# Kernel optimization log

Hardware: AMD Instinct MI355X
Metric: run time of the kernel (lower is better)

## Reference

```python
import jax, jax.numpy as jnp
import numpy as np

N, D, NUM_CLASSES = 8192, 256, 64
MARGIN_SAME = 0.9
MARGIN_DIFF = 0.5


def setup_inputs() -> dict:
    key = jax.random.key(0)
    k1, k2 = jax.random.split(key)
    inputs = jax.random.normal(k1, (N, D), dtype=jnp.float32)
    # contrastive losses with cosine-style margins expect unit-norm embeddings
    inputs = inputs / jnp.linalg.norm(inputs, axis=1, keepdims=True)
    targets = jax.random.randint(k2, (N,), 0, NUM_CLASSES, dtype=jnp.int64)
    return {"inputs": inputs, "targets": targets}


def reference(inputs, targets):
    n = inputs.shape[0]
    sim = jnp.matmul(inputs, inputs.T)  # [n, n] pairwise similarities

    same = targets[:, None] == targets[None, :]  # [n, n]
    pos_mask = same & (sim < 1.0)                # pos_pair_ selection per row
    neg_mask = ~same                             # neg_pair_ selection per row

    pos_active = pos_mask & (sim < MARGIN_SAME)  # contribute 1 - sim
    neg_active = neg_mask & (sim > MARGIN_DIFF)  # contribute sim

    # sum over all rows, divided by n (sort in the original is irrelevant to sums)
    loss = (jnp.sum(jnp.where(pos_active, 1.0 - sim, 0.0))
            + jnp.sum(jnp.where(neg_active, sim, 0.0))) / n

    prec = jnp.float32(0.0)  # original: c is never incremented

    # original reports means of the LAST row's pos_pair_ / neg_pair_
    last_sim = sim[n - 1]
    lp = pos_mask[n - 1]
    ln = neg_mask[n - 1]
    mean_pos_sim = jnp.sum(jnp.where(lp, last_sim, 0.0)) / jnp.maximum(
        jnp.sum(lp).astype(jnp.float32), 1.0)
    mean_neg_sim = jnp.sum(jnp.where(ln, last_sim, 0.0)) / jnp.maximum(
        jnp.sum(ln).astype(jnp.float32), 1.0)

    return (loss, prec, mean_pos_sim, mean_neg_sim)
```

## Files before the change

kernel.cpp:

```cpp
#include <hip/hip_runtime.h>
#include <hip/hip_bf16.h>

#define N_ 8192
#define D_ 256
#define BM 128
#define BK 32
#define NB (N_ / BM)
#define NT (NB * (NB + 1) / 2)
#define KSTEPS (D_ / BK)

typedef __bf16 bf16x8 __attribute__((ext_vector_type(8)));
typedef float f32x4 __attribute__((ext_vector_type(4)));

__global__ void cvt_kernel(const float4* __restrict__ in, ushort4* __restrict__ out, int n4,
                           double* __restrict__ accd) {
  int i = blockIdx.x * blockDim.x + threadIdx.x;
  if (blockIdx.x == 0 && threadIdx.x < 128) accd[threadIdx.x] = 0.0;
  if (i >= n4) return;
  float4 v = in[i];
  union { __hip_bfloat16 h[4]; ushort4 u; } t;
  t.h[0] = __float2bfloat16(v.x);
  t.h[1] = __float2bfloat16(v.y);
  t.h[2] = __float2bfloat16(v.z);
  t.h[3] = __float2bfloat16(v.w);
  out[i] = t.u;
}

__global__ __launch_bounds__(256, 3) void simloss_kernel(
    const __hip_bfloat16* __restrict__ Xb, const int* __restrict__ tg,
    double* __restrict__ accd) {
  __shared__ __align__(16) char lds[3 * 16384];

  const int t0 = blockIdx.x;
  const int t = (t0 & 7) * (NT / 8) + (t0 >> 3);

  int bi = (int)(((2.0f * NB + 1.0f) -
                  sqrtf((2.0f * NB + 1.0f) * (2.0f * NB + 1.0f) - 8.0f * (float)t)) * 0.5f);
  if (bi < 0) bi = 0;
  if (bi > NB - 1) bi = NB - 1;
  while (((bi + 1) * NB - ((bi + 1) * bi) / 2) <= t) ++bi;
  while ((bi * NB - (bi * (bi - 1)) / 2) > t) --bi;
  const int bj = bi + (t - (bi * NB - (bi * (bi - 1)) / 2));

  const int tid = threadIdx.x;
  const int lane = tid & 63, wv = tid >> 6;
  const int wr = wv >> 1, wc = wv & 1;
  const int rowA0 = bi * BM, rowB0 = bj * BM;

  const int c0 = (wv * 2 + 0) * 64 + lane;
  const int c1 = (wv * 2 + 1) * 64 + lane;
  const int r0 = c0 >> 2, s0 = (c0 & 3) ^ ((r0 >> 1) & 3);
  const int r1 = c1 >> 2, s1 = (c1 & 3) ^ ((r1 >> 1) & 3);
  const __hip_bfloat16* gA0 = Xb + (size_t)(rowA0 + r0) * D_ + s0 * 8;
  const __hip_bfloat16* gA1 = Xb + (size_t)(rowA0 + r1) * D_ + s1 * 8;
  const __hip_bfloat16* gB0 = Xb + (size_t)(rowB0 + r0) * D_ + s0 * 8;
  const __hip_bfloat16* gB1 = Xb + (size_t)(rowB0 + r1) * D_ + s1 * 8;

#define GLDS(g, l) \
  __builtin_amdgcn_global_load_lds((const __attribute__((address_space(1))) void*)(g), \
                                   (__attribute__((address_space(3))) void*)(l), 16, 0, 0)
#define STAGE(buf, kt)                                    \
  do {                                                    \
    char* base = lds + (buf) * 16384;                     \
    GLDS(gA0 + (kt) * BK, base + c0 * 16);                \
    GLDS(gA1 + (kt) * BK, base + c1 * 16);                \
    GLDS(gB0 + (kt) * BK, base + 8192 + c0 * 16);         \
    GLDS(gB1 + (kt) * BK, base + 8192 + c1 * 16);         \
  } while (0)

  const int fr = lane & 15, sl = lane >> 4;
  const int rswz = sl ^ ((fr >> 1) & 3);
  const int aoff = (wr * 64 + fr) * 64 + rswz * 16;
  const int boff = (wc * 64 + fr) * 64 + rswz * 16;

  f32x4 acc[4][4] = {};

  STAGE(0, 0);
  STAGE(1, 1);
  STAGE(2, 2);

#pragma unroll
  for (int kt = 0; kt < KSTEPS; ++kt) {
    if (kt < 6)
      asm volatile("s_waitcnt vmcnt(8)" ::: "memory");
    else if (kt == 6)
      asm volatile("s_waitcnt vmcnt(4)" ::: "memory");
    else
      asm volatile("s_waitcnt vmcnt(0)" ::: "memory");
    __builtin_amdgcn_s_barrier();

    const char* Ab = lds + (kt % 3) * 16384;
    const char* Bb = Ab + 8192;
    bf16x8 af[4], bfr[4];
#pragma unroll
    for (int m = 0; m < 4; ++m) af[m] = *(const bf16x8*)(Ab + aoff + m * 1024);
#pragma unroll
    for (int n = 0; n < 4; ++n) bfr[n] = *(const bf16x8*)(Bb + boff + n * 1024);
#pragma unroll
    for (int m = 0; m < 4; ++m)
#pragma unroll
      for (int n = 0; n < 4; ++n)
        acc[m][n] = __builtin_amdgcn_mfma_f32_16x16x32_bf16(af[m], bfr[n], acc[m][n], 0, 0, 0);

    asm volatile("s_waitcnt lgkmcnt(0)" ::: "memory");
    __builtin_amdgcn_sched_barrier(0);
    __builtin_amdgcn_s_barrier();
    if (kt + 3 < KSTEPS) STAGE(kt % 3, kt + 3);
  }
#undef STAGE
#undef GLDS

  const int cRow = sl * 4, cCol = fr;
  int tj[4], ti[4][4];
#pragma unroll
  for (int n = 0; n < 4; ++n) tj[n] = tg[rowB0 + wc * 64 + n * 16 + cCol];
#pragma unroll
  for (int m = 0; m < 4; ++m)
#pragma unroll
    for (int r = 0; r < 4; ++r) ti[m][r] = tg[rowA0 + wr * 64 + m * 16 + cRow + r];

  float pc = 0.f, ps = 0.f, ns = 0.f;
#pragma unroll
  for (int m = 0; m < 4; ++m)
#pragma unroll
    for (int n = 0; n < 4; ++n)
#pragma unroll
      for (int r = 0; r < 4; ++r) {
        float s = acc[m][n][r];
        bool same = (ti[m][r] == tj[n]);
        if (same & (s < 0.9f)) { pc += 1.0f; ps += s; }
        if ((!same) & (s > 0.5f)) { ns += s; }
      }

  if (bj == NB - 1 && wc == 1 && cCol == 15) {
    const int tlast = tj[3];
    float lps = 0.f, lns = 0.f, lpc = 0.f, lnc = 0.f;
#pragma unroll
    for (int m = 0; m < 4; ++m)
#pragma unroll
      for (int r = 0; r < 4; ++r) {
        float s = acc[m][3][r];
        bool same = (ti[m][r] == tlast);
        if (same && s < 1.0f) { lps += s; lpc += 1.f; }
        if (!same) { lns += s; lnc += 1.f; }
      }
    atomicAdd(&accd[96], (double)lps);
    atomicAdd(&accd[97], (double)lpc);
    atomicAdd(&accd[98], (double)lns);
    atomicAdd(&accd[99], (double)lnc);
  }

#pragma unroll
  for (int off = 32; off > 0; off >>= 1) {
    pc += __shfl_down(pc, off);
    ps += __shfl_down(ps, off);
    ns += __shfl_down(ns, off);
  }
  float* red = (float*)lds;
  if (lane == 0) { red[0 + wv] = pc; red[4 + wv] = ps; red[8 + wv] = ns; }
  __syncthreads();
  if (tid == 0) {
    double w = (bi == bj) ? 1.0 : 2.0;
    double* slot = accd + (blockIdx.x & 31) * 3;
    atomicAdd(&slot[0], w * (double)(red[0] + red[1] + red[2] + red[3]));
    atomicAdd(&slot[1], w * (double)(red[4] + red[5] + red[6] + red[7]));
    atomicAdd(&slot[2], w * (double)(red[8] + red[9] + red[10] + red[11]));
  }
}

__global__ void finalize_kernel(const double* __restrict__ accd, float* __restrict__ out) {
  double pc = 0.0, ps = 0.0, ns = 0.0;
#pragma unroll
  for (int i = 0; i < 32; ++i) {
    pc += accd[i * 3 + 0];
    ps += accd[i * 3 + 1];
    ns += accd[i * 3 + 2];
  }
  double loss = (pc - ps + ns) / (double)N_;
  out[0] = (float)loss;
  out[1] = 0.0f;
  out[2] = (float)(accd[96] / fmax(accd[97], 1.0));
  out[3] = (float)(accd[98] / fmax(accd[99], 1.0));
}

extern "C" void kernel_launch(void* const* d_in, const int* in_sizes, int n_in,
                              void* d_out, int out_size, void* d_ws, size_t ws_size,
                              hipStream_t stream) {
  const float* X = (const float*)d_in[0];
  const int* tg = (const int*)d_in[1];
  float* out = (float*)d_out;
  double* accd = (double*)d_ws;
  __hip_bfloat16* Xb = (__hip_bfloat16*)((char*)d_ws + 1024);

  int n4 = N_ * D_ / 4;
  cvt_kernel<<<(n4 + 255) / 256, 256, 0, stream>>>((const float4*)X, (ushort4*)Xb, n4, accd);

  simloss_kernel<<<NT, 256, 0, stream>>>(Xb, tg, accd);

  finalize_kernel<<<1, 1, 0, stream>>>(accd, out);
}
```

Before: 39.99 us.

## Enlarge symmetric Gram tiles to 256x256 with 512-thread blocks

Doubles the block tile from 128x128 to 256x256 and uses 8 waves per block, each computing a 64x128 sub-tile with 4x8 MFMA accumulators. The aim is higher arithmetic intensity per staged byte and fewer blocks (528 instead of 2080) along with fewer reduction atomics. In exchange, per-thread register use and the LDS footprint (96KB) grow. Fewer, larger blocks may also cause tail imbalance across CUs.

```diff
diff --git a/kernel.cpp b/kernel.cpp
--- a/kernel.cpp
+++ b/kernel.cpp
@@ -3,10 +3,10 @@
 
 #define N_ 8192
 #define D_ 256
-#define BM 128
+#define BM 256
 #define BK 32
-#define NB (N_ / BM)
-#define NT (NB * (NB + 1) / 2)
+#define NB2 (N_ / BM)
+#define NT2 (NB2 * (NB2 + 1) / 2)
 #define KSTEPS (D_ / BK)
 
 typedef __bf16 bf16x8 __attribute__((ext_vector_type(8)));
@@ -26,29 +26,29 @@
   out[i] = t.u;
 }
 
-__global__ __launch_bounds__(256, 3) void simloss_kernel(
+__global__ __launch_bounds__(512, 2) void simloss_kernel(
     const __hip_bfloat16* __restrict__ Xb, const int* __restrict__ tg,
     double* __restrict__ accd) {
-  __shared__ __align__(16) char lds[3 * 16384];
+  __shared__ __align__(16) char lds[3 * 32768];
 
   const int t0 = blockIdx.x;
-  const int t = (t0 & 7) * (NT / 8) + (t0 >> 3);
-
-  int bi = (int)(((2.0f * NB + 1.0f) -
-                  sqrtf((2.0f * NB + 1.0f) * (2.0f * NB + 1.0f) - 8.0f * (float)t)) * 0.5f);
+  const int t = (t0 & 7) * (NT2 / 8) + (t0 >> 3);
+
+  int bi = (int)(((2.0f * NB2 + 1.0f) -
+                  sqrtf((2.0f * NB2 + 1.0f) * (2.0f * NB2 + 1.0f) - 8.0f * (float)t)) * 0.5f);
   if (bi < 0) bi = 0;
-  if (bi > NB - 1) bi = NB - 1;
-  while (((bi + 1) * NB - ((bi + 1) * bi) / 2) <= t) ++bi;
-  while ((bi * NB - (bi * (bi - 1)) / 2) > t) --bi;
-  const int bj = bi + (t - (bi * NB - (bi * (bi - 1)) / 2));
+  if (bi > NB2 - 1) bi = NB2 - 1;
+  while (((bi + 1) * NB2 - ((bi + 1) * bi) / 2) <= t) ++bi;
+  while ((bi * NB2 - (bi * (bi - 1)) / 2) > t) --bi;
+  const int bj = bi + (t - (bi * NB2 - (bi * (bi - 1)) / 2));
 
   const int tid = threadIdx.x;
   const int lane = tid & 63, wv = tid >> 6;
-  const int wr = wv >> 1, wc = wv & 1;
+  const int wrow = wv >> 1, wcol = wv & 1;
   const int rowA0 = bi * BM, rowB0 = bj * BM;
 
-  const int c0 = (wv * 2 + 0) * 64 + lane;
-  const int c1 = (wv * 2 + 1) * 64 + lane;
+  const int c0 = wv * 128 + lane;
+  const int c1 = c0 + 64;
   const int r0 = c0 >> 2, s0 = (c0 & 3) ^ ((r0 >> 1) & 3);
   const int r1 = c1 >> 2, s1 = (c1 & 3) ^ ((r1 >> 1) & 3);
   const __hip_bfloat16* gA0 = Xb + (size_t)(rowA0 + r0) * D_ + s0 * 8;
@@ -61,19 +61,19 @@
                                    (__attribute__((address_space(3))) void*)(l), 16, 0, 0)
 #define STAGE(buf, kt)                                    \
   do {                                                    \
-    char* base = lds + (buf) * 16384;                     \
+    char* base = lds + (buf) * 32768;                     \
     GLDS(gA0 + (kt) * BK, base + c0 * 16);                \
     GLDS(gA1 + (kt) * BK, base + c1 * 16);                \
-    GLDS(gB0 + (kt) * BK, base + 8192 + c0 * 16);         \
-    GLDS(gB1 + (kt) * BK, base + 8192 + c1 * 16);         \
+    GLDS(gB0 + (kt) * BK, base + 16384 + c0 * 16);        \
+    GLDS(gB1 + (kt) * BK, base + 16384 + c1 * 16);        \
   } while (0)
 
   const int fr = lane & 15, sl = lane >> 4;
   const int rswz = sl ^ ((fr >> 1) & 3);
-  const int aoff = (wr * 64 + fr) * 64 + rswz * 16;
-  const int boff = (wc * 64 + fr) * 64 + rswz * 16;
-
-  f32x4 acc[4][4] = {};
+  const int aoff = (wrow * 64 + fr) * 64 + rswz * 16;
+  const int boff = 16384 + (wcol * 128 + fr) * 64 + rswz * 16;
+
+  f32x4 acc[4][8] = {};
 
   STAGE(0, 0);
   STAGE(1, 1);
@@ -89,17 +89,16 @@
       asm volatile("s_waitcnt vmcnt(0)" ::: "memory");
     __builtin_amdgcn_s_barrier();
 
-    const char* Ab = lds + (kt % 3) * 16384;
-    const char* Bb = Ab + 8192;
-    bf16x8 af[4], bfr[4];
+    const char* Ab = lds + (kt % 3) * 32768;
+    bf16x8 af[4], bfr[8];
 #pragma unroll
     for (int m = 0; m < 4; ++m) af[m] = *(const bf16x8*)(Ab + aoff + m * 1024);
 #pragma unroll
-    for (int n = 0; n < 4; ++n) bfr[n] = *(const bf16x8*)(Bb + boff + n * 1024);
+    for (int n = 0; n < 8; ++n) bfr[n] = *(const bf16x8*)(Ab + boff + n * 1024);
 #pragma unroll
     for (int m = 0; m < 4; ++m)
 #pragma unroll
-      for (int n = 0; n < 4; ++n)
+      for (int n = 0; n < 8; ++n)
         acc[m][n] = __builtin_amdgcn_mfma_f32_16x16x32_bf16(af[m], bfr[n], acc[m][n], 0, 0, 0);
 
     asm volatile("s_waitcnt lgkmcnt(0)" ::: "memory");
@@ -111,19 +110,19 @@
 #undef GLDS
 
   const int cRow = sl * 4, cCol = fr;
-  int tj[4], ti[4][4];
-#pragma unroll
-  for (int n = 0; n < 4; ++n) tj[n] = tg[rowB0 + wc * 64 + n * 16 + cCol];
+  int tj[8], ti[4][4];
+#pragma unroll
+  for (int n = 0; n < 8; ++n) tj[n] = tg[rowB0 + wcol * 128 + n * 16 + cCol];
 #pragma unroll
   for (int m = 0; m < 4; ++m)
 #pragma unroll
-    for (int r = 0; r < 4; ++r) ti[m][r] = tg[rowA0 + wr * 64 + m * 16 + cRow + r];
+    for (int r = 0; r < 4; ++r) ti[m][r] = tg[rowA0 + wrow * 64 + m * 16 + cRow + r];
 
   float pc = 0.f, ps = 0.f, ns = 0.f;
 #pragma unroll
   for (int m = 0; m < 4; ++m)
 #pragma unroll
-    for (int n = 0; n < 4; ++n)
+    for (int n = 0; n < 8; ++n)
 #pragma unroll
       for (int r = 0; r < 4; ++r) {
         float s = acc[m][n][r];
@@ -132,14 +131,14 @@
         if ((!same) & (s > 0.5f)) { ns += s; }
       }
 
-  if (bj == NB - 1 && wc == 1 && cCol == 15) {
-    const int tlast = tj[3];
+  if (bj == NB2 - 1 && wcol == 1 && cCol == 15) {
+    const int tlast = tj[7];
     float lps = 0.f, lns = 0.f, lpc = 0.f, lnc = 0.f;
 #pragma unroll
     for (int m = 0; m < 4; ++m)
 #pragma unroll
       for (int r = 0; r < 4; ++r) {
-        float s = acc[m][3][r];
+        float s = acc[m][7][r];
         bool same = (ti[m][r] == tlast);
         if (same && s < 1.0f) { lps += s; lpc += 1.f; }
         if (!same) { lns += s; lnc += 1.f; }
@@ -157,14 +156,17 @@
     ns += __shfl_down(ns, off);
   }
   float* red = (float*)lds;
-  if (lane == 0) { red[0 + wv] = pc; red[4 + wv] = ps; red[8 + wv] = ns; }
+  if (lane == 0) { red[0 + wv] = pc; red[8 + wv] = ps; red[16 + wv] = ns; }
   __syncthreads();
   if (tid == 0) {
+    float rpc = 0.f, rps = 0.f, rns = 0.f;
+#pragma unroll
+    for (int q = 0; q < 8; ++q) { rpc += red[q]; rps += red[8 + q]; rns += red[16 + q]; }
     double w = (bi == bj) ? 1.0 : 2.0;
     double* slot = accd + (blockIdx.x & 31) * 3;
-    atomicAdd(&slot[0], w * (double)(red[0] + red[1] + red[2] + red[3]));
-    atomicAdd(&slot[1], w * (double)(red[4] + red[5] + red[6] + red[7]));
-    atomicAdd(&slot[2], w * (double)(red[8] + red[9] + red[10] + red[11]));
+    atomicAdd(&slot[0], w * (double)rpc);
+    atomicAdd(&slot[1], w * (double)rps);
+    atomicAdd(&slot[2], w * (double)rns);
   }
 }
 
@@ -195,7 +197,7 @@
   int n4 = N_ * D_ / 4;
   cvt_kernel<<<(n4 + 255) / 256, 256, 0, stream>>>((const float4*)X, (ushort4*)Xb, n4, accd);
 
-  simloss_kernel<<<NT, 256, 0, stream>>>(Xb, tg, accd);
+  simloss_kernel<<<NT2, 512, 0, stream>>>(Xb, tg, accd);
 
   finalize_kernel<<<1, 1, 0, stream>>>(accd, out);
 }
```

Result: slower. 49.37 us (+23.5%).
